# Optimization experiments

Hardware: AMD Instinct MI355X
Metric: run time of the kernel (lower is better)

The kernel has to match this reference:

```python
import jax, jax.numpy as jnp
import numpy as np

SEGMENT_LENGTHS = [1024, 2048, 4096]
DILATION_RATES = [1, 2, 4]


def _head_groups(num_heads, num_segments):
    base = num_heads // num_segments
    extra = num_heads % num_segments
    groups = [base] * num_segments
    for i in range(extra):
        groups[-(i + 1)] += 1
    return groups


def _dilated_indices(segment_len, dilation_rate, offset):
    # Mirrors RingDilatedAttentionV2._apply_dilation index construction (static).
    if dilation_rate > 1:
        idx = np.arange(offset, segment_len, dilation_rate)
        repeats = (segment_len + len(idx) - 1) // len(idx)
        idx = np.tile(idx, repeats)[:segment_len] % segment_len
    else:
        idx = np.arange(segment_len)
    return jnp.asarray(idx, dtype=jnp.int32)


def setup_inputs() -> dict:
    key = jax.random.key(0)
    kq, kk, kv = jax.random.split(key, 3)
    b, n, h, d = 1, 4096, 12, 64
    return {
        "query": jax.random.normal(kq, (b, n, h, d), dtype=jnp.float32),
        "key": jax.random.normal(kk, (b, n, h, d), dtype=jnp.float32),
        "value": jax.random.normal(kv, (b, n, h, d), dtype=jnp.float32),
        "is_causal": 1,
    }


def _dilated_attention(query, key, value, is_causal):
    b, n, h, d = query.shape
    groups = _head_groups(h, len(SEGMENT_LENGTHS))
    scale = 1.0 / np.sqrt(d).astype(np.float32)
    outs = []
    head_start = 0
    for i, (seg_len, rate, g) in enumerate(zip(SEGMENT_LENGTHS, DILATION_RATES, groups)):
        if g == 0:
            continue
        sl = min(seg_len, n)
        ns = n // sl  # n chosen divisible by every segment length
        q = query[:, :, head_start:head_start + g, :].reshape(b, ns, sl, g, d)
        k = key[:, :, head_start:head_start + g, :].reshape(b, ns, sl, g, d)
        v = value[:, :, head_start:head_start + g, :].reshape(b, ns, sl, g, d)
        if rate > 1 or i > 0:
            idx = _dilated_indices(sl, rate, i)
            k = k[:, :, idx]
            v = v[:, :, idx]
        # scores: [b, seg, heads, q_pos, k_pos]
        scores = jnp.einsum("bsqhd,bskhd->bshqk", q, k) * scale
        if is_causal:
            causal = jnp.triu(jnp.ones((sl, sl), dtype=bool), k=1)
            scores = jnp.where(causal, jnp.finfo(scores.dtype).min, scores)
        attn = jax.nn.softmax(scores, axis=-1)
        o = jnp.einsum("bshqk,bskhd->bsqhd", attn, v).reshape(b, n, g, d)
        outs.append(o)
        head_start += g
    return jnp.concatenate(outs, axis=2)  # [b, n, h, d]


def reference(query, key, value, is_causal):
    return _dilated_attention(query, key, value, is_causal)
```

## Files before the change

### kernel.cpp

```cpp
#include <hip/hip_runtime.h>
#include <hip/hip_bf16.h>
#include <math.h>

typedef __bf16 bf16x8 __attribute__((ext_vector_type(8)));
typedef float  f32x4  __attribute__((ext_vector_type(4)));
typedef float  f32x16 __attribute__((ext_vector_type(16)));
typedef int    int2v  __attribute__((ext_vector_type(2)));
typedef unsigned int uint4v __attribute__((ext_vector_type(4)));
typedef unsigned short ushort_t;

#define LDK 72

#define KG_OFF  0
#define VGT_OFF 6291456
#define LACC_OFF 12582912
#define CTR_OFF  12779520

struct ItemTab { unsigned short v[896]; int n; };

constexpr ItemTab build_items(int causal) {
    ItemTab t{};
    for (int i = 0; i < 896; ++i) t.v[i] = 0xFFFF;
    t.n = 0;
    for (int cost = 16; cost >= 1; --cost)
        for (int qt = 31; qt >= 0; --qt)
            for (int h = 11; h >= 0; --h) {
                const int group = h >> 2;
                const int sl = 1024 << group;
                const int qb = (qt << 7) & (sl - 1);
                const int nkt = causal ? (((qb + 127) >> 6) + 1) : (sl >> 6);
                for (int c = 0; c < 4; ++c) {
                    const int kt0 = c << 4;
                    if (kt0 >= nkt) continue;
                    const int rem = nkt - kt0;
                    const int cst = rem < 16 ? rem : 16;
                    if (cst == cost) t.v[t.n++] = (unsigned short)((qt << 6) | (h << 2) | c);
                }
            }
    return t;
}

__constant__ ItemTab g_tab_c = build_items(1);
__constant__ ItemTab g_tab_n = build_items(0);

__device__ __forceinline__ int gather_pos(int gi, int group) {
    const int lsl = 10 + group;
    const int seg = gi >> lsl;
    const int j   = gi - (seg << lsl);
    return (seg << lsl) + group + ((j & 1023) << group);
}

__device__ __forceinline__ void gld_lds16(const ushort_t* g, __bf16* l) {
    __builtin_amdgcn_global_load_lds(
        (const __attribute__((address_space(1))) void*)g,
        (__attribute__((address_space(3))) void*)l, 16, 0, 0);
}

__device__ __forceinline__ unsigned int pk_bf16(float lo, float hi) {
    unsigned short a = __builtin_bit_cast(unsigned short, (__bf16)lo);
    unsigned short b = __builtin_bit_cast(unsigned short, (__bf16)hi);
    return ((unsigned int)b << 16) | (unsigned int)a;
}

__device__ __forceinline__ f32x16 zero16() {
    f32x16 z;
    #pragma unroll
    for (int i = 0; i < 16; ++i) z[i] = 0.f;
    return z;
}

__global__ __launch_bounds__(256)
void preconvert_kernel(const float* __restrict__ K, const float* __restrict__ V,
                       ushort_t* __restrict__ Kg, ushort_t* __restrict__ VgT,
                       float* __restrict__ Out, float* __restrict__ l_acc,
                       int* __restrict__ ctr, const int* __restrict__ is_causal_p)
{
    const int HD = 768;
    int b = blockIdx.x;
    const int tid = threadIdx.x;
    if (b < 768) {
        if (b == 0 && tid == 0) *ctr = 0;
        {
            const int causal = (*is_causal_p) != 0;
            const int rh = (b * 256 + tid) >> 2;
            const int h_ = rh % 12;
            const int row_ = rh / 12;
            const int grp = h_ >> 2;
            const int ntf = 16 << grp;
            const int qt128 = row_ >> 7;
            const int qb_t = (qt128 << 1) & (ntf - 1);
            const int nkt = causal ? (qb_t + 2) : ntf;
            if (nkt > 16) {
                float4 z = {0.f, 0.f, 0.f, 0.f};
                float4* zp = (float4*)Out + ((size_t)b * 256 + tid) * 4;
                zp[0] = z; zp[1] = z; zp[2] = z; zp[3] = z;
            }
        }
        const int h = b % 12, gi0 = (b / 12) * 64;
        const int group = h >> 2;
        const int gi = gi0 + (tid >> 2);
        const int d0 = (tid & 3) << 4;
        const int pos = gather_pos(gi, group);
        const float* kp = K + (size_t)pos * HD + h * 64 + d0;
        float4 x0 = ((const float4*)kp)[0], x1 = ((const float4*)kp)[1];
        float4 x2 = ((const float4*)kp)[2], x3 = ((const float4*)kp)[3];
        bf16x8 w0, w1;
        w0[0]=(__bf16)x0.x; w0[1]=(__bf16)x0.y; w0[2]=(__bf16)x0.z; w0[3]=(__bf16)x0.w;
        w0[4]=(__bf16)x1.x; w0[5]=(__bf16)x1.y; w0[6]=(__bf16)x1.z; w0[7]=(__bf16)x1.w;
        w1[0]=(__bf16)x2.x; w1[1]=(__bf16)x2.y; w1[2]=(__bf16)x2.z; w1[3]=(__bf16)x2.w;
        w1[4]=(__bf16)x3.x; w1[5]=(__bf16)x3.y; w1[6]=(__bf16)x3.z; w1[7]=(__bf16)x3.w;
        ushort_t* out = Kg + ((size_t)(h * 4096 + gi)) * 64 + d0;
        *(bf16x8*)out = w0;
        *(bf16x8*)(out + 8) = w1;
    } else {
        b -= 768;
        if (b < 192) l_acc[b * 256 + tid] = 0.f;
        const int h = b % 12, gi0 = (b / 12) * 64;
        const int group = h >> 2;
        __shared__ __align__(16) __bf16 Ts[64 * LDK];
        const int gil = tid >> 2;
        const int d0 = (tid & 3) << 4;
        const int pos = gather_pos(gi0 + gil, group);
        const float* vp = V + (size_t)pos * HD + h * 64 + d0;
        float4 x0 = ((const float4*)vp)[0], x1 = ((const float4*)vp)[1];
        float4 x2 = ((const float4*)vp)[2], x3 = ((const float4*)vp)[3];
        bf16x8 w0, w1;
        w0[0]=(__bf16)x0.x; w0[1]=(__bf16)x0.y; w0[2]=(__bf16)x0.z; w0[3]=(__bf16)x0.w;
        w0[4]=(__bf16)x1.x; w0[5]=(__bf16)x1.y; w0[6]=(__bf16)x1.z; w0[7]=(__bf16)x1.w;
        w1[0]=(__bf16)x2.x; w1[1]=(__bf16)x2.y; w1[2]=(__bf16)x2.z; w1[3]=(__bf16)x2.w;
        w1[4]=(__bf16)x3.x; w1[5]=(__bf16)x3.y; w1[6]=(__bf16)x3.z; w1[7]=(__bf16)x3.w;
        *(bf16x8*)&Ts[gil * LDK + d0]     = w0;
        *(bf16x8*)&Ts[gil * LDK + d0 + 8] = w1;
        __syncthreads();
        const int d = tid >> 2, c = tid & 3;
        bf16x8 o0, o1;
        #pragma unroll
        for (int i = 0; i < 8; ++i) {
            o0[i] = Ts[(c * 16 + i) * LDK + d];
            o1[i] = Ts[(c * 16 + 8 + i) * LDK + d];
        }
        ushort_t* out = VgT + ((size_t)(h * 64 + d)) * 4096 + gi0 + c * 16;
        *(bf16x8*)out = o0;
        *(bf16x8*)(out + 8) = o1;
    }
}

__global__ __launch_bounds__(256)
void dilated_attn_kernel(const float* __restrict__ Q,
                         const ushort_t* __restrict__ Kg,
                         const ushort_t* __restrict__ VgT,
                         const int* __restrict__ is_causal_p,
                         float* __restrict__ Out,
                         float* __restrict__ l_acc,
                         int* __restrict__ ctr)
{
    const int HD = 768;
    const int causal = (*is_causal_p) != 0;
    const ItemTab& tab = causal ? g_tab_c : g_tab_n;
    const int n_items = tab.n;

    const int tid  = threadIdx.x;
    const int wave = tid >> 6;
    const int lane = tid & 63;
    const int l31  = lane & 31;
    const int hi   = lane >> 5;

    __shared__ __align__(16) __bf16 Ks[4][64 * 64];
    __shared__ __align__(16) __bf16 Vs[4][64 * 64];
    __shared__ int s_item;

    const int bx16 = (((lane & 7) ^ (lane >> 3)) & 7) << 3;
    const int r8   = lane >> 3;

    for (;;) {
        if (tid == 0) s_item = atomicAdd(ctr, 1);
        __syncthreads();
        const int n = s_item;
        __syncthreads();
        if (n >= n_items) break;

        const int enc = tab.v[n];
        const int qt  = enc >> 6;
        const int h   = (enc >> 2) & 15;
        const int c   = enc & 3;
        const int group = h >> 2;
        const int sl    = 1024 << group;

        const int q0 = qt << 7;
        const int qb = q0 & (sl - 1);
        const int seg_start = q0 - qb;
        const int blk_diag = (qb + 127) >> 6;
        const int nkt = causal ? (blk_diag + 1) : (sl >> 6);
        const int kt0 = c << 4;
        const int kend = min(kt0 + 16, nkt);
        const int nch  = (nkt + 15) >> 4;

        const ushort_t* kg_head = Kg + (size_t)h * 4096 * 64;
        const ushort_t* vt_head = VgT + (size_t)h * 64 * 4096;

        auto stage = [&](int kt, int buf) {
            const ushort_t* kb = kg_head + ((size_t)(seg_start + (kt << 6)) << 6);
            const ushort_t* vb = vt_head + seg_start + (kt << 6);
            #pragma unroll
            for (int i = 0; i < 2; ++i) {
                const int row = i * 32 + wave * 8 + r8;
                gld_lds16(kb + row * 64 + bx16, &Ks[buf][(i * 32 + wave * 8) * 64]);
                gld_lds16(vb + (size_t)row * 4096 + bx16, &Vs[buf][(i * 32 + wave * 8) * 64]);
            }
        };

        const int qrow = q0 + wave * 32 + l31;
        const float* qptr = Q + (size_t)qrow * HD + h * 64;
        float4 xq[8];
        #pragma unroll
        for (int ds = 0; ds < 4; ++ds) {
            xq[ds * 2]     = ((const float4*)(qptr + ds * 16 + hi * 8))[0];
            xq[ds * 2 + 1] = ((const float4*)(qptr + ds * 16 + hi * 8))[1];
        }
        stage(kt0, 0);
        stage(min(kt0 + 1, kend - 1), 1);
        stage(min(kt0 + 2, kend - 1), 2);

        bf16x8 qf[4];
        {
            const float s = 0.125f * 1.4426950408889634f;
            #pragma unroll
            for (int ds = 0; ds < 4; ++ds) {
                float4 x0 = xq[ds * 2], x1 = xq[ds * 2 + 1];
                bf16x8 w;
                w[0]=(__bf16)(x0.x*s); w[1]=(__bf16)(x0.y*s); w[2]=(__bf16)(x0.z*s); w[3]=(__bf16)(x0.w*s);
                w[4]=(__bf16)(x1.x*s); w[5]=(__bf16)(x1.y*s); w[6]=(__bf16)(x1.z*s); w[7]=(__bf16)(x1.w*s);
                qf[ds] = w;
            }
        }

        const int mydiag = causal ? ((qb + wave * 32 + 31) >> 6) : 0x7fffffff;
        const int lrow   = ((wave & 1) << 5) + l31;

        f32x16 o0 = zero16(), o1 = zero16();
        float l_part = 0.f;

        for (int kt = kt0; kt < kend; ++kt) {
            const int cur = (kt - kt0) & 3;

            asm volatile("s_waitcnt vmcnt(8)" ::: "memory");
            __builtin_amdgcn_s_barrier();
            __builtin_amdgcn_sched_barrier(0);

            stage(min(kt + 3, kend - 1), (cur + 3) & 3);

            if (kt <= mydiag) {
                f32x16 s0 = zero16(), s1 = zero16();
                const int xr = (l31 & 7);
                __builtin_amdgcn_s_setprio(1);
                #pragma unroll
                for (int ds = 0; ds < 4; ++ds) {
                    const int cb = ds * 2 + hi;
                    bf16x8 k0 = *(const bf16x8*)&Ks[cur][l31 * 64        + ((cb ^ xr) << 3)];
                    bf16x8 k1 = *(const bf16x8*)&Ks[cur][(32 + l31) * 64 + ((cb ^ xr) << 3)];
                    s0 = __builtin_amdgcn_mfma_f32_32x32x16_bf16(k0, qf[ds], s0, 0, 0, 0);
                    s1 = __builtin_amdgcn_mfma_f32_32x32x16_bf16(k1, qf[ds], s1, 0, 0, 0);
                }
                __builtin_amdgcn_s_setprio(0);

                float p[2][16];
                const bool isdiag = causal && (kt == mydiag);
                #pragma unroll
                for (int r = 0; r < 16; ++r) {
                    float v0 = __builtin_amdgcn_exp2f(s0[r]);
                    float v1 = __builtin_amdgcn_exp2f(s1[r]);
                    if (isdiag) {
                        const int kl = (r & 3) + ((r >> 2) << 3) + (hi << 2);
                        if (kl > lrow)      v0 = 0.f;
                        if (kl + 32 > lrow) v1 = 0.f;
                    }
                    p[0][r] = v0; p[1][r] = v1;
                    l_part += v0 + v1;
                }

                __builtin_amdgcn_s_setprio(1);
                #pragma unroll
                for (int b = 0; b < 2; ++b) {
                    #pragma unroll
                    for (int ks2 = 0; ks2 < 2; ++ks2) {
                        const int g = ks2 * 8;
                        int x0 = (int)pk_bf16(p[b][g + 0], p[b][g + 1]);
                        int x1 = (int)pk_bf16(p[b][g + 2], p[b][g + 3]);
                        int y0 = (int)pk_bf16(p[b][g + 4], p[b][g + 5]);
                        int y1 = (int)pk_bf16(p[b][g + 6], p[b][g + 7]);
                        int2v r02 = __builtin_amdgcn_permlane32_swap(x0, y0, false, false);
                        int2v r13 = __builtin_amdgcn_permlane32_swap(x1, y1, false, false);
                        uint4v t;
                        t[0] = (unsigned int)r02[0];
                        t[1] = (unsigned int)r13[0];
                        t[2] = (unsigned int)r02[1];
                        t[3] = (unsigned int)r13[1];
                        bf16x8 pa = __builtin_bit_cast(bf16x8, t);
                        const int kcb = (b * 2 + ks2) * 2 + hi;
                        bf16x8 v0 = *(const bf16x8*)&Vs[cur][l31 * 64        + ((kcb ^ xr) << 3)];
                        bf16x8 v1 = *(const bf16x8*)&Vs[cur][(32 + l31) * 64 + ((kcb ^ xr) << 3)];
                        o0 = __builtin_amdgcn_mfma_f32_32x32x16_bf16(pa, v0, o0, 0, 0, 0);
                        o1 = __builtin_amdgcn_mfma_f32_32x32x16_bf16(pa, v1, o1, 0, 0, 0);
                    }
                }
                __builtin_amdgcn_s_setprio(0);
            }
        }

        const float l2 = l_part + __shfl_xor(l_part, 32);
        const int qw = q0 + wave * 32;
        if (nch == 1) {
            const float inv = 1.0f / l2;
            #pragma unroll
            for (int r = 0; r < 16; ++r) {
                const int qloc = (r & 3) + ((r >> 2) << 3) + (hi << 2);
                const float invq = __shfl(inv, qloc);
                const int row = qw + qloc;
                Out[(size_t)row * HD + h * 64 + l31]      = o0[r] * invq;
                Out[(size_t)row * HD + h * 64 + 32 + l31] = o1[r] * invq;
            }
        } else {
            if (hi == 0) atomicAdd(&l_acc[(qw + l31) * 12 + h], l2);
            #pragma unroll
            for (int r = 0; r < 16; ++r) {
                const int qloc = (r & 3) + ((r >> 2) << 3) + (hi << 2);
                const int row = qw + qloc;
                atomicAdd(&Out[(size_t)row * HD + h * 64 + l31],      o0[r]);
                atomicAdd(&Out[(size_t)row * HD + h * 64 + 32 + l31], o1[r]);
            }
        }
    }
}

__global__ __launch_bounds__(256)
void finalize_kernel(float* __restrict__ Out, const float* __restrict__ l_acc,
                     const int* __restrict__ is_causal_p)
{
    const int causal = (*is_causal_p) != 0;
    const int idx = blockIdx.x * 256 + threadIdx.x;
    const int rh = idx >> 4;
    const int d4 = idx & 15;
    const int h = rh % 12;
    const int row = rh / 12;
    const int group = h >> 2;
    const int ntf = 16 << group;
    const int qt128 = row >> 7;
    const int qb_t = (qt128 << 1) & (ntf - 1);
    const int nkt = causal ? (qb_t + 2) : ntf;
    if (nkt <= 16) return;
    const float inv = 1.0f / l_acc[rh];
    float4* p = (float4*)Out + (size_t)rh * 16 + d4;
    float4 v = *p;
    v.x *= inv; v.y *= inv; v.z *= inv; v.w *= inv;
    *p = v;
}

extern "C" void kernel_launch(void* const* d_in, const int* in_sizes, int n_in,
                              void* d_out, int out_size, void* d_ws, size_t ws_size,
                              hipStream_t stream) {
    (void)in_sizes; (void)n_in; (void)out_size; (void)ws_size;
    const float* Q = (const float*)d_in[0];
    const float* K = (const float*)d_in[1];
    const float* V = (const float*)d_in[2];
    const int* isc = (const int*)d_in[3];
    float* Out = (float*)d_out;
    ushort_t* Kg   = (ushort_t*)((char*)d_ws + KG_OFF);
    ushort_t* VgT  = (ushort_t*)((char*)d_ws + VGT_OFF);
    float*    lacc = (float*)((char*)d_ws + LACC_OFF);
    int*      ctr  = (int*)((char*)d_ws + CTR_OFF);

    preconvert_kernel<<<1536, 256, 0, stream>>>(K, V, Kg, VgT, Out, lacc, ctr, isc);
    dilated_attn_kernel<<<512, 256, 0, stream>>>(Q, Kg, VgT, isc, Out, lacc, ctr);
    finalize_kernel<<<3072, 256, 0, stream>>>(Out, lacc, isc);
}
```

Baseline: 133.1 us.

## Replace direct-to-LDS async loads with register-staged double buffering and more blocks

```diff
diff --git a/kernel.cpp b/kernel.cpp
--- a/kernel.cpp
+++ b/kernel.cpp
@@ -48,12 +48,6 @@
     const int seg = gi >> lsl;
     const int j   = gi - (seg << lsl);
     return (seg << lsl) + group + ((j & 1023) << group);
-}
-
-__device__ __forceinline__ void gld_lds16(const ushort_t* g, __bf16* l) {
-    __builtin_amdgcn_global_load_lds(
-        (const __attribute__((address_space(1))) void*)g,
-        (__attribute__((address_space(3))) void*)l, 16, 0, 0);
 }
 
 __device__ __forceinline__ unsigned int pk_bf16(float lo, float hi) {
@@ -96,22 +90,32 @@
                 zp[0] = z; zp[1] = z; zp[2] = z; zp[3] = z;
             }
         }
-        const int h = b % 12, gi0 = (b / 12) * 64;
+        const int h = b % 12, p0 = (b / 12) * 64;
         const int group = h >> 2;
-        const int gi = gi0 + (tid >> 2);
+        const int pos = p0 + (tid >> 2);
         const int d0 = (tid & 3) << 4;
-        const int pos = gather_pos(gi, group);
-        const float* kp = K + (size_t)pos * HD + h * 64 + d0;
-        float4 x0 = ((const float4*)kp)[0], x1 = ((const float4*)kp)[1];
-        float4 x2 = ((const float4*)kp)[2], x3 = ((const float4*)kp)[3];
-        bf16x8 w0, w1;
-        w0[0]=(__bf16)x0.x; w0[1]=(__bf16)x0.y; w0[2]=(__bf16)x0.z; w0[3]=(__bf16)x0.w;
-        w0[4]=(__bf16)x1.x; w0[5]=(__bf16)x1.y; w0[6]=(__bf16)x1.z; w0[7]=(__bf16)x1.w;
-        w1[0]=(__bf16)x2.x; w1[1]=(__bf16)x2.y; w1[2]=(__bf16)x2.z; w1[3]=(__bf16)x2.w;
-        w1[4]=(__bf16)x3.x; w1[5]=(__bf16)x3.y; w1[6]=(__bf16)x3.z; w1[7]=(__bf16)x3.w;
-        ushort_t* out = Kg + ((size_t)(h * 4096 + gi)) * 64 + d0;
-        *(bf16x8*)out = w0;
-        *(bf16x8*)(out + 8) = w1;
+        const int lsl = 10 + group;
+        const int rate = 1 << group;
+        const int seg_base = (pos >> lsl) << lsl;
+        const int po = pos - seg_base;
+        const int rem = po - group;
+        if (rem >= 0 && (rem & (rate - 1)) == 0) {
+            const float* kp = K + (size_t)pos * HD + h * 64 + d0;
+            float4 x0 = ((const float4*)kp)[0], x1 = ((const float4*)kp)[1];
+            float4 x2 = ((const float4*)kp)[2], x3 = ((const float4*)kp)[3];
+            bf16x8 w0, w1;
+            w0[0]=(__bf16)x0.x; w0[1]=(__bf16)x0.y; w0[2]=(__bf16)x0.z; w0[3]=(__bf16)x0.w;
+            w0[4]=(__bf16)x1.x; w0[5]=(__bf16)x1.y; w0[6]=(__bf16)x1.z; w0[7]=(__bf16)x1.w;
+            w1[0]=(__bf16)x2.x; w1[1]=(__bf16)x2.y; w1[2]=(__bf16)x2.z; w1[3]=(__bf16)x2.w;
+            w1[4]=(__bf16)x3.x; w1[5]=(__bf16)x3.y; w1[6]=(__bf16)x3.z; w1[7]=(__bf16)x3.w;
+            const int jb = rem >> group;
+            for (int k = 0; k < rate; ++k) {
+                const int gi = seg_base + jb + (k << 10);
+                ushort_t* out = Kg + ((size_t)(h * 4096 + gi)) * 64 + d0;
+                *(bf16x8*)out = w0;
+                *(bf16x8*)(out + 8) = w1;
+            }
+        }
     } else {
         b -= 768;
         if (b < 192) l_acc[b * 256 + tid] = 0.f;
@@ -145,7 +149,7 @@
     }
 }
 
-__global__ __launch_bounds__(256)
+__global__ __launch_bounds__(256, 4)
 void dilated_attn_kernel(const float* __restrict__ Q,
                          const ushort_t* __restrict__ Kg,
                          const ushort_t* __restrict__ VgT,
@@ -165,12 +169,14 @@
     const int l31  = lane & 31;
     const int hi   = lane >> 5;
 
-    __shared__ __align__(16) __bf16 Ks[4][64 * 64];
-    __shared__ __align__(16) __bf16 Vs[4][64 * 64];
+    __shared__ __align__(16) __bf16 Ks[2][64 * 64];
+    __shared__ __align__(16) __bf16 Vs[2][64 * 64];
     __shared__ int s_item;
 
-    const int bx16 = (((lane & 7) ^ (lane >> 3)) & 7) << 3;
-    const int r8   = lane >> 3;
+    const int r8    = lane >> 3;
+    const int c8    = lane & 7;
+    const int col16 = c8 << 3;
+    const int wcol  = ((c8 ^ r8) << 3);
 
     for (;;) {
         if (tid == 0) s_item = atomicAdd(ctr, 1);
@@ -198,15 +204,22 @@
         const ushort_t* kg_head = Kg + (size_t)h * 4096 * 64;
         const ushort_t* vt_head = VgT + (size_t)h * 64 * 4096;
 
-        auto stage = [&](int kt, int buf) {
+        uint4v kr0, kr1, vr0, vr1;
+        auto load_tile = [&](int kt) {
             const ushort_t* kb = kg_head + ((size_t)(seg_start + (kt << 6)) << 6);
             const ushort_t* vb = vt_head + seg_start + (kt << 6);
-            #pragma unroll
-            for (int i = 0; i < 2; ++i) {
-                const int row = i * 32 + wave * 8 + r8;
-                gld_lds16(kb + row * 64 + bx16, &Ks[buf][(i * 32 + wave * 8) * 64]);
-                gld_lds16(vb + (size_t)row * 4096 + bx16, &Vs[buf][(i * 32 + wave * 8) * 64]);
-            }
+            const int row0 = wave * 8 + r8;
+            kr0 = *(const uint4v*)(kb + row0 * 64 + col16);
+            kr1 = *(const uint4v*)(kb + (row0 + 32) * 64 + col16);
+            vr0 = *(const uint4v*)(vb + (size_t)row0 * 4096 + col16);
+            vr1 = *(const uint4v*)(vb + (size_t)(row0 + 32) * 4096 + col16);
+        };
+        auto write_tile = [&](int buf) {
+            const int row0 = wave * 8 + r8;
+            *(uint4v*)&Ks[buf][row0 * 64 + wcol]        = kr0;
+            *(uint4v*)&Ks[buf][(row0 + 32) * 64 + wcol] = kr1;
+            *(uint4v*)&Vs[buf][row0 * 64 + wcol]        = vr0;
+            *(uint4v*)&Vs[buf][(row0 + 32) * 64 + wcol] = vr1;
         };
 
         const int qrow = q0 + wave * 32 + l31;
@@ -217,9 +230,7 @@
             xq[ds * 2]     = ((const float4*)(qptr + ds * 16 + hi * 8))[0];
             xq[ds * 2 + 1] = ((const float4*)(qptr + ds * 16 + hi * 8))[1];
         }
-        stage(kt0, 0);
-        stage(min(kt0 + 1, kend - 1), 1);
-        stage(min(kt0 + 2, kend - 1), 2);
+        load_tile(kt0);
 
         bf16x8 qf[4];
         {
@@ -241,13 +252,14 @@
         float l_part = 0.f;
 
         for (int kt = kt0; kt < kend; ++kt) {
-            const int cur = (kt - kt0) & 3;
-
-            asm volatile("s_waitcnt vmcnt(8)" ::: "memory");
+            const int cur = (kt - kt0) & 1;
+
+            write_tile(cur);
+            if (kt + 1 < kend) load_tile(kt + 1);
+
+            asm volatile("s_waitcnt lgkmcnt(0)" ::: "memory");
             __builtin_amdgcn_s_barrier();
             __builtin_amdgcn_sched_barrier(0);
-
-            stage(min(kt + 3, kend - 1), (cur + 3) & 3);
 
             if (kt <= mydiag) {
                 f32x16 s0 = zero16(), s1 = zero16();
@@ -370,6 +382,6 @@
     int*      ctr  = (int*)((char*)d_ws + CTR_OFF);
 
     preconvert_kernel<<<1536, 256, 0, stream>>>(K, V, Kg, VgT, Out, lacc, ctr, isc);
-    dilated_attn_kernel<<<512, 256, 0, stream>>>(Q, Kg, VgT, isc, Out, lacc, ctr);
+    dilated_attn_kernel<<<1024, 256, 0, stream>>>(Q, Kg, VgT, isc, Out, lacc, ctr);
     finalize_kernel<<<3072, 256, 0, stream>>>(Out, lacc, isc);
 }
```

New measurement: 139.3 us. 1.05x slower.
